# Performance work log

Hardware: AMD Instinct MI355X
Metric: run time of the kernel (lower is better)

## Reference

```python
import jax, jax.numpy as jnp
import numpy as np
import math

INPUT_SIZE = 4096
NUM_NEURONS = 4096
ATTN_SIZE = 64
BATCH = 8192


def setup_inputs() -> dict:
    key = jax.random.key(0)
    ks = jax.random.split(key, 10)
    lim_in = 1.0 / math.sqrt(INPUT_SIZE)
    lim_a = 1.0 / math.sqrt(ATTN_SIZE)
    x = jax.random.normal(ks[0], (BATCH, INPUT_SIZE), dtype=jnp.float32)
    # attention linears (torch default uniform(-1/sqrt(fan_in), ...))
    Wq = jax.random.uniform(ks[1], (ATTN_SIZE, INPUT_SIZE), jnp.float32, -lim_in, lim_in)
    bq = jnp.zeros((ATTN_SIZE,), jnp.float32)
    Wk = jax.random.uniform(ks[2], (ATTN_SIZE, INPUT_SIZE), jnp.float32, -lim_in, lim_in)
    bk = jnp.zeros((ATTN_SIZE,), jnp.float32)
    Wv = jax.random.uniform(ks[3], (ATTN_SIZE, INPUT_SIZE), jnp.float32, -lim_in, lim_in)
    bv = jnp.zeros((ATTN_SIZE,), jnp.float32)
    Wo = jax.random.uniform(ks[4], (INPUT_SIZE, ATTN_SIZE), jnp.float32, -lim_a, lim_a)
    bo = jnp.zeros((INPUT_SIZE,), jnp.float32)
    # stacked single-weight neurons: weight ~ N(0,1)*0.01, bias 0
    Wn = jax.random.normal(ks[5], (NUM_NEURONS, INPUT_SIZE), jnp.float32) * 0.01
    bn = jnp.zeros((NUM_NEURONS,), jnp.float32)
    return {"x": x, "Wq": Wq, "bq": bq, "Wk": Wk, "bk": bk,
            "Wv": Wv, "bv": bv, "Wo": Wo, "bo": bo, "Wn": Wn, "bn": bn}


def reference(x, Wq, bq, Wk, bk, Wv, bv, Wo, bo, Wn, bn):
    scale = math.sqrt(ATTN_SIZE)
    # x is treated as a length-1 "sequence" of the full feature vector: [B, 1, S]
    q = x @ Wq.T + bq            # [B, A]
    k = x @ Wk.T + bk            # [B, A]
    v = x @ Wv.T + bv            # [B, A]
    # attention over a single token: softmax of a single score == 1, kept for fidelity
    scores = jnp.sum(q * k, axis=-1, keepdims=True) / scale      # [B, 1]
    attn_w = jax.nn.softmax(scores[:, :, None], axis=-1)          # [B, 1, 1] -> all ones
    attended = attn_w[:, 0, :] * v                                # [B, A] == v
    attn_out = attended @ Wo.T + bo                               # [B, S]
    h = attn_out + x                                              # residual
    # stacked single-weight neurons == one GEMM
    out = h @ Wn.T + bn                                           # [B, N]
    return jax.nn.relu(out)
```

## Files before the change

kernel.cpp:

```cpp
#include <hip/hip_runtime.h>
#include <stdint.h>


typedef unsigned short u16;
typedef float f32x4 __attribute__((ext_vector_type(4)));
typedef __bf16 bf16x8 __attribute__((ext_vector_type(8)));
typedef u16 u16x8 __attribute__((ext_vector_type(8)));

__device__ __forceinline__ float b2f(u16 u) {
  union { unsigned int i; float f; } x; x.i = ((unsigned int)u) << 16; return x.f;
}
__device__ __forceinline__ u16 f2b(float f) {
  union { float f; unsigned int i; } x; x.f = f;
  unsigned int r = x.i + 0x7FFFu + ((x.i >> 16) & 1u);
  return (u16)(r >> 16);
}

__device__ __forceinline__ void gl_lds16(const u16* g, u16* l) {
#if __has_builtin(__builtin_amdgcn_global_load_lds)
  __builtin_amdgcn_global_load_lds((__attribute__((address_space(1))) void*)g,
                                   (__attribute__((address_space(3))) void*)l, 16, 0, 0);
#else
  int lane = threadIdx.x & 63;
  *(u16x8*)(l + lane * 8) = *(const u16x8*)g;
#endif
}

__device__ __forceinline__ f32x4 mfma16(bf16x8 a, bf16x8 b, f32x4 c) {
  return __builtin_amdgcn_mfma_f32_16x16x32_bf16(a, b, c, 0, 0, 0);
}

#define XCH 4194304L
#define WNCH 2097152L
__global__ __launch_bounds__(256) void k_cvt(
    const float* __restrict__ x, const float* __restrict__ Wn, const float* __restrict__ Wv,
    u16* __restrict__ xb, u16* __restrict__ Wnb, u16* __restrict__ Wvb) {
  long i = (long)blockIdx.x * 256 + threadIdx.x;
  const float* src; u16* dst; long off;
  if (i < XCH) { src = x; dst = xb; off = i * 8; }
  else if (i < XCH + WNCH) { src = Wn; dst = Wnb; off = (i - XCH) * 8; }
  else { src = Wv; dst = Wvb; off = (i - XCH - WNCH) * 8; }
  f32x4 a = *(const f32x4*)&src[off];
  f32x4 b = *(const f32x4*)&src[off + 4];
  u16x8 o;
#pragma unroll
  for (int e = 0; e < 4; ++e) { o[e] = f2b(a[e]); o[4 + e] = f2b(b[e]); }
  *(u16x8*)&dst[off] = o;
}

__global__ __launch_bounds__(256) void kT(const float* __restrict__ Wo, u16* __restrict__ WoT) {
  __shared__ __align__(16) u16 t[64 * 72];
  const int b = blockIdx.x;
  const int tid = threadIdx.x;
  {
    int k = tid >> 2, a0 = (tid & 3) * 16;
    const float* src = &Wo[(size_t)(b * 64 + k) * 64 + a0];
#pragma unroll
    for (int q = 0; q < 4; ++q) {
      f32x4 v = *(const f32x4*)&src[q * 4];
#pragma unroll
      for (int e = 0; e < 4; ++e) t[k * 72 + a0 + q * 4 + e] = f2b(v[e]);
    }
  }
  __syncthreads();
  {
    int a = tid >> 2, k0 = (tid & 3) * 16;
    u16x8 o0, o1;
#pragma unroll
    for (int j = 0; j < 8; ++j) o0[j] = t[(k0 + j) * 72 + a];
#pragma unroll
    for (int j = 0; j < 8; ++j) o1[j] = t[(k0 + 8 + j) * 72 + a];
    *(u16x8*)&WoT[(size_t)a * 4096 + b * 64 + k0] = o0;
    *(u16x8*)&WoT[(size_t)a * 4096 + b * 64 + k0 + 8] = o1;
  }
}

#define PBK 128
__device__ void gemm_n64(const u16* __restrict__ A, const u16* __restrict__ B,
                         u16* __restrict__ C, const float* __restrict__ bias,
                         long m0, u16* lA, u16* lB) {
  const int tid = threadIdx.x;
  const int w = tid >> 6, l = tid & 63;
  f32x4 acc[4];
#pragma unroll
  for (int nt = 0; nt < 4; ++nt) acc[nt] = (f32x4)(0.f);

  for (int k0 = 0; k0 < 4096; k0 += PBK) {
    __syncthreads();
#pragma unroll
    for (int i = 0; i < 4; ++i) {
      int row = w * 16 + i * 4 + (l >> 4);
      int p = (l & 15) ^ (i * 4 + (l >> 4));
      gl_lds16(A + (m0 + row) * (long)4096 + k0 + p * 8, lA + (w * 16 + i * 4) * PBK);
      gl_lds16(B + (long)row * 4096 + k0 + p * 8, lB + (w * 16 + i * 4) * PBK);
    }
    __syncthreads();
#pragma unroll
    for (int kk = 0; kk < 4; ++kk) {
      int slotA = ((kk * 4 + (l >> 4)) ^ (l & 15)) * 8;
      bf16x8 af = *(const bf16x8*)&lA[(w * 16 + (l & 15)) * PBK + slotA];
#pragma unroll
      for (int nt = 0; nt < 4; ++nt) {
        bf16x8 bf = *(const bf16x8*)&lB[(nt * 16 + (l & 15)) * PBK + slotA];
        acc[nt] = mfma16(af, bf, acc[nt]);
      }
    }
  }
#pragma unroll
  for (int nt = 0; nt < 4; ++nt) {
    int col = nt * 16 + (l & 15);
    float bb = bias ? bias[col] : 0.f;
#pragma unroll
    for (int r = 0; r < 4; ++r) {
      long row = m0 + w * 16 + (l >> 4) * 4 + r;
      C[row * 64 + col] = f2b(acc[nt][r] + bb);
    }
  }
}

__global__ __launch_bounds__(256, 2) void k_prep(
    const u16* __restrict__ xb, const u16* __restrict__ Wvb, const float* __restrict__ bv,
    const u16* __restrict__ Wnb, const u16* __restrict__ WoT,
    const float* __restrict__ bo, const float* __restrict__ bn,
    u16* __restrict__ V, u16* __restrict__ Wm, float* __restrict__ biasTot) {
  __shared__ __align__(16) u16 lA[64 * PBK];
  __shared__ __align__(16) u16 lB[64 * PBK];
  const int bid = blockIdx.x;
  if (bid < 128) {
    gemm_n64(xb, Wvb, V, bv, (long)bid * 64, lA, lB);
  } else if (bid < 192) {
    gemm_n64(Wnb, WoT, Wm, nullptr, (long)(bid - 128) * 64, lA, lB);
  } else {
    const int w = threadIdx.x >> 6, l = threadIdx.x & 63;
    const int n = (bid - 192) * 4 + w;
    float s = 0.f;
#pragma unroll
    for (int j = 0; j < 8; ++j) {
      int off = (j * 64 + l) * 8;
      u16x8 a = *(const u16x8*)&Wnb[(size_t)n * 4096 + off];
      f32x4 c0 = *(const f32x4*)&bo[off];
      f32x4 c1 = *(const f32x4*)&bo[off + 4];
#pragma unroll
      for (int e = 0; e < 4; ++e) s += b2f(a[e]) * c0[e] + b2f(a[4 + e]) * c1[e];
    }
#pragma unroll
    for (int o = 32; o > 0; o >>= 1) s += __shfl_xor(s, o, 64);
    if (l == 0) biasTot[n] = s + bn[n];
  }
}

__global__ __launch_bounds__(256, 2) void k_main(
    const u16* __restrict__ X, const u16* __restrict__ Wn,
    const u16* __restrict__ V, const u16* __restrict__ Wm,
    const float* __restrict__ biasTot, float* __restrict__ Out) {
  __shared__ __align__(16) u16 smem[2 * 128 * 64];
  u16* lA = smem;
  u16* lB = smem + 128 * 64;
  const int tid = threadIdx.x;
  const int w = tid >> 6, l = tid & 63;
  const int wRow = (w & 1) * 64, wCol = (w >> 1) * 64;
  const long mBase = (long)(blockIdx.x >> 5) * 128;
  const int nBase = (int)(blockIdx.x & 31) * 128;

  f32x4 acc[4][4];
#pragma unroll
  for (int mt = 0; mt < 4; ++mt)
#pragma unroll
    for (int nt = 0; nt < 4; ++nt) acc[mt][nt] = (f32x4)(0.f);

  const int srow = l >> 3;
  const int sp = ((l & 7) ^ srow) * 8;

  for (int kb = 0; kb < 65; ++kb) {
    const u16 *pA, *pB; long lda;
    if (kb < 64) { pA = X + (long)kb * 64; pB = Wn + (long)kb * 64; lda = 4096; }
    else         { pA = V;                 pB = Wm;                 lda = 64;  }
    __syncthreads();
#pragma unroll
    for (int i = 0; i < 4; ++i) {
      int row = w * 32 + i * 8 + srow;
      gl_lds16(pA + (mBase + row) * lda + sp, lA + (w * 32 + i * 8) * 64);
      gl_lds16(pB + (long)(nBase + row) * lda + sp, lB + (w * 32 + i * 8) * 64);
    }
    __syncthreads();
#pragma unroll
    for (int kk = 0; kk < 2; ++kk) {
      int slot = ((kk * 4 + (l >> 4)) ^ (l & 7)) * 8;
      bf16x8 af[4], bfr[4];
#pragma unroll
      for (int mt = 0; mt < 4; ++mt)
        af[mt] = *(const bf16x8*)&lA[(wRow + mt * 16 + (l & 15)) * 64 + slot];
#pragma unroll
      for (int nt = 0; nt < 4; ++nt)
        bfr[nt] = *(const bf16x8*)&lB[(wCol + nt * 16 + (l & 15)) * 64 + slot];
#pragma unroll
      for (int mt = 0; mt < 4; ++mt)
#pragma unroll
        for (int nt = 0; nt < 4; ++nt) acc[mt][nt] = mfma16(af[mt], bfr[nt], acc[mt][nt]);
    }
  }

  __syncthreads();
  float* eb = ((float*)smem) + w * 1024;
#pragma unroll
  for (int mt = 0; mt < 4; ++mt) {
#pragma unroll
    for (int nt = 0; nt < 4; ++nt) {
      float bt = biasTot[nBase + wCol + nt * 16 + (l & 15)];
#pragma unroll
      for (int r = 0; r < 4; ++r) {
        float val = acc[mt][nt][r] + bt;
        eb[((l >> 4) * 4 + r) * 64 + nt * 16 + (l & 15)] = fmaxf(val, 0.f);
      }
    }
    int rr = l >> 2, c0 = (l & 3) * 16;
    long grow = mBase + wRow + mt * 16 + rr;
    int gcol = nBase + wCol + c0;
    f32x4 o0 = *(const f32x4*)&eb[rr * 64 + c0];
    f32x4 o1 = *(const f32x4*)&eb[rr * 64 + c0 + 4];
    f32x4 o2 = *(const f32x4*)&eb[rr * 64 + c0 + 8];
    f32x4 o3 = *(const f32x4*)&eb[rr * 64 + c0 + 12];
    *(f32x4*)&Out[grow * 4096 + gcol] = o0;
    *(f32x4*)&Out[grow * 4096 + gcol + 4] = o1;
    *(f32x4*)&Out[grow * 4096 + gcol + 8] = o2;
    *(f32x4*)&Out[grow * 4096 + gcol + 12] = o3;
  }
}

extern "C" void kernel_launch(void* const* d_in, const int* in_sizes, int n_in,
                              void* d_out, int out_size, void* d_ws, size_t ws_size,
                              hipStream_t stream) {
  const float* x  = (const float*)d_in[0];
  const float* Wv = (const float*)d_in[5];
  const float* bv = (const float*)d_in[6];
  const float* Wo = (const float*)d_in[7];
  const float* bo = (const float*)d_in[8];
  const float* Wn = (const float*)d_in[9];
  const float* bn = (const float*)d_in[10];
  float* out = (float*)d_out;

  char* ws = (char*)d_ws;
  u16* xb  = (u16*)ws;
  u16* Wnb = (u16*)(ws + (64L << 20));
  u16* Wvb = (u16*)(ws + (96L << 20));
  u16* WoT = (u16*)(ws + (96L << 20) + (512 << 10));
  u16* V   = (u16*)(ws + (97L << 20));
  u16* Wm  = (u16*)(ws + (98L << 20));
  float* biasTot = (float*)(ws + (98L << 20) + (512 << 10));

  k_cvt<<<dim3(24704), dim3(256), 0, stream>>>(x, Wn, Wv, xb, Wnb, Wvb);
  kT<<<dim3(64), dim3(256), 0, stream>>>(Wo, WoT);
  k_prep<<<dim3(1216), dim3(256), 0, stream>>>(xb, Wvb, bv, Wnb, WoT, bo, bn, V, Wm, biasTot);
  k_main<<<dim3(2048), dim3(256), 0, stream>>>(xb, Wnb, V, Wm, biasTot, out);
}
```

Measured before the change: 605.9 us.

## Materialize residual h in bf16 instead of folding Wo into Wn

Drops the Wm = Wn·Wo precompute and the extra K=64 block in the main GEMM. Instead it computes V with a split-K kernel that converts x and Wv in-kernel, writing fp32 partials into the output buffer. It then builds h = V·Wo^T + bo + x in bf16 and runs the main GEMM on h with only bn as bias. This removes the separate x conversion pass and the Wn·WoT GEMM, but adds an extra bf16 write and read of h and rounds h to bf16 rather than x.

```diff
diff --git a/kernel.cpp b/kernel.cpp
--- a/kernel.cpp
+++ b/kernel.cpp
@@ -7,9 +7,6 @@
 typedef __bf16 bf16x8 __attribute__((ext_vector_type(8)));
 typedef u16 u16x8 __attribute__((ext_vector_type(8)));
 
-__device__ __forceinline__ float b2f(u16 u) {
-  union { unsigned int i; float f; } x; x.i = ((unsigned int)u) << 16; return x.f;
-}
 __device__ __forceinline__ u16 f2b(float f) {
   union { float f; unsigned int i; } x; x.f = f;
   unsigned int r = x.i + 0x7FFFu + ((x.i >> 16) & 1u);
@@ -30,129 +27,158 @@
   return __builtin_amdgcn_mfma_f32_16x16x32_bf16(a, b, c, 0, 0, 0);
 }
 
-#define XCH 4194304L
-#define WNCH 2097152L
-__global__ __launch_bounds__(256) void k_cvt(
-    const float* __restrict__ x, const float* __restrict__ Wn, const float* __restrict__ Wv,
-    u16* __restrict__ xb, u16* __restrict__ Wnb, u16* __restrict__ Wvb) {
-  long i = (long)blockIdx.x * 256 + threadIdx.x;
-  const float* src; u16* dst; long off;
-  if (i < XCH) { src = x; dst = xb; off = i * 8; }
-  else if (i < XCH + WNCH) { src = Wn; dst = Wnb; off = (i - XCH) * 8; }
-  else { src = Wv; dst = Wvb; off = (i - XCH - WNCH) * 8; }
-  f32x4 a = *(const f32x4*)&src[off];
-  f32x4 b = *(const f32x4*)&src[off + 4];
-  u16x8 o;
-#pragma unroll
-  for (int e = 0; e < 4; ++e) { o[e] = f2b(a[e]); o[4 + e] = f2b(b[e]); }
-  *(u16x8*)&dst[off] = o;
-}
-
-__global__ __launch_bounds__(256) void kT(const float* __restrict__ Wo, u16* __restrict__ WoT) {
-  __shared__ __align__(16) u16 t[64 * 72];
-  const int b = blockIdx.x;
-  const int tid = threadIdx.x;
-  {
-    int k = tid >> 2, a0 = (tid & 3) * 16;
-    const float* src = &Wo[(size_t)(b * 64 + k) * 64 + a0];
-#pragma unroll
-    for (int q = 0; q < 4; ++q) {
-      f32x4 v = *(const f32x4*)&src[q * 4];
-#pragma unroll
-      for (int e = 0; e < 4; ++e) t[k * 72 + a0 + q * 4 + e] = f2b(v[e]);
-    }
-  }
-  __syncthreads();
-  {
-    int a = tid >> 2, k0 = (tid & 3) * 16;
-    u16x8 o0, o1;
-#pragma unroll
-    for (int j = 0; j < 8; ++j) o0[j] = t[(k0 + j) * 72 + a];
-#pragma unroll
-    for (int j = 0; j < 8; ++j) o1[j] = t[(k0 + 8 + j) * 72 + a];
-    *(u16x8*)&WoT[(size_t)a * 4096 + b * 64 + k0] = o0;
-    *(u16x8*)&WoT[(size_t)a * 4096 + b * 64 + k0 + 8] = o1;
-  }
-}
-
-#define PBK 128
-__device__ void gemm_n64(const u16* __restrict__ A, const u16* __restrict__ B,
-                         u16* __restrict__ C, const float* __restrict__ bias,
-                         long m0, u16* lA, u16* lB) {
+__device__ __forceinline__ void cvt16(const float* s, u16* d0, u16* d1) {
+  f32x4 a0 = *(const f32x4*)s, a1 = *(const f32x4*)(s + 4);
+  f32x4 a2 = *(const f32x4*)(s + 8), a3 = *(const f32x4*)(s + 12);
+  u16x8 o0, o1;
+#pragma unroll
+  for (int e = 0; e < 4; ++e) { o0[e] = f2b(a0[e]); o0[4 + e] = f2b(a1[e]); }
+#pragma unroll
+  for (int e = 0; e < 4; ++e) { o1[e] = f2b(a2[e]); o1[4 + e] = f2b(a3[e]); }
+  *(u16x8*)d0 = o0; *(u16x8*)d1 = o1;
+}
+
+__global__ __launch_bounds__(256, 2) void k_v(
+    const float* __restrict__ x, const float* __restrict__ Wv, float* __restrict__ Vp) {
+  __shared__ __align__(16) u16 lA[64 * 72];
+  __shared__ __align__(16) u16 lB[64 * 72];
   const int tid = threadIdx.x;
   const int w = tid >> 6, l = tid & 63;
+  const long m0 = (long)(blockIdx.x >> 2) * 64;
+  const int kbase = (int)(blockIdx.x & 3) * 1024;
   f32x4 acc[4];
 #pragma unroll
   for (int nt = 0; nt < 4; ++nt) acc[nt] = (f32x4)(0.f);
 
-  for (int k0 = 0; k0 < 4096; k0 += PBK) {
-    __syncthreads();
-#pragma unroll
-    for (int i = 0; i < 4; ++i) {
-      int row = w * 16 + i * 4 + (l >> 4);
-      int p = (l & 15) ^ (i * 4 + (l >> 4));
-      gl_lds16(A + (m0 + row) * (long)4096 + k0 + p * 8, lA + (w * 16 + i * 4) * PBK);
-      gl_lds16(B + (long)row * 4096 + k0 + p * 8, lB + (w * 16 + i * 4) * PBK);
-    }
-    __syncthreads();
-#pragma unroll
-    for (int kk = 0; kk < 4; ++kk) {
-      int slotA = ((kk * 4 + (l >> 4)) ^ (l & 15)) * 8;
-      bf16x8 af = *(const bf16x8*)&lA[(w * 16 + (l & 15)) * PBK + slotA];
+  const int srow = tid >> 2, sc = (tid & 3) * 16;
+  for (int it = 0; it < 16; ++it) {
+    const int k0 = kbase + it * 64;
+    __syncthreads();
+    cvt16(&x[(m0 + srow) * 4096 + k0 + sc], &lA[srow * 72 + sc], &lA[srow * 72 + sc + 8]);
+    cvt16(&Wv[(long)srow * 4096 + k0 + sc], &lB[srow * 72 + sc], &lB[srow * 72 + sc + 8]);
+    __syncthreads();
+#pragma unroll
+    for (int kk = 0; kk < 2; ++kk) {
+      const int ko = kk * 32 + (l >> 4) * 8;
+      bf16x8 af = *(const bf16x8*)&lA[(w * 16 + (l & 15)) * 72 + ko];
 #pragma unroll
       for (int nt = 0; nt < 4; ++nt) {
-        bf16x8 bf = *(const bf16x8*)&lB[(nt * 16 + (l & 15)) * PBK + slotA];
+        bf16x8 bf = *(const bf16x8*)&lB[(nt * 16 + (l & 15)) * 72 + ko];
         acc[nt] = mfma16(af, bf, acc[nt]);
       }
     }
   }
+  const long ksoff = (long)(blockIdx.x & 3) * 8192;
 #pragma unroll
   for (int nt = 0; nt < 4; ++nt) {
     int col = nt * 16 + (l & 15);
-    float bb = bias ? bias[col] : 0.f;
 #pragma unroll
     for (int r = 0; r < 4; ++r) {
       long row = m0 + w * 16 + (l >> 4) * 4 + r;
-      C[row * 64 + col] = f2b(acc[nt][r] + bb);
-    }
-  }
-}
-
-__global__ __launch_bounds__(256, 2) void k_prep(
-    const u16* __restrict__ xb, const u16* __restrict__ Wvb, const float* __restrict__ bv,
-    const u16* __restrict__ Wnb, const u16* __restrict__ WoT,
-    const float* __restrict__ bo, const float* __restrict__ bn,
-    u16* __restrict__ V, u16* __restrict__ Wm, float* __restrict__ biasTot) {
-  __shared__ __align__(16) u16 lA[64 * PBK];
-  __shared__ __align__(16) u16 lB[64 * PBK];
-  const int bid = blockIdx.x;
-  if (bid < 128) {
-    gemm_n64(xb, Wvb, V, bv, (long)bid * 64, lA, lB);
-  } else if (bid < 192) {
-    gemm_n64(Wnb, WoT, Wm, nullptr, (long)(bid - 128) * 64, lA, lB);
-  } else {
-    const int w = threadIdx.x >> 6, l = threadIdx.x & 63;
-    const int n = (bid - 192) * 4 + w;
-    float s = 0.f;
-#pragma unroll
-    for (int j = 0; j < 8; ++j) {
-      int off = (j * 64 + l) * 8;
-      u16x8 a = *(const u16x8*)&Wnb[(size_t)n * 4096 + off];
-      f32x4 c0 = *(const f32x4*)&bo[off];
-      f32x4 c1 = *(const f32x4*)&bo[off + 4];
-#pragma unroll
-      for (int e = 0; e < 4; ++e) s += b2f(a[e]) * c0[e] + b2f(a[4 + e]) * c1[e];
-    }
-#pragma unroll
-    for (int o = 32; o > 0; o >>= 1) s += __shfl_xor(s, o, 64);
-    if (l == 0) biasTot[n] = s + bn[n];
+      Vp[(ksoff + row) * 64 + col] = acc[nt][r];
+    }
+  }
+}
+
+__global__ __launch_bounds__(256) void k_cvtWn(const float* __restrict__ Wn,
+                                               u16* __restrict__ Wnb) {
+  long off = ((long)blockIdx.x * 256 + threadIdx.x) * 8;
+  f32x4 a = *(const f32x4*)&Wn[off];
+  f32x4 b = *(const f32x4*)&Wn[off + 4];
+  u16x8 o;
+#pragma unroll
+  for (int e = 0; e < 4; ++e) { o[e] = f2b(a[e]); o[4 + e] = f2b(b[e]); }
+  *(u16x8*)&Wnb[off] = o;
+}
+
+__global__ __launch_bounds__(256, 3) void k_h(
+    const float* __restrict__ x, const float* __restrict__ Wo,
+    const float* __restrict__ bv, const float* __restrict__ bo,
+    const float* __restrict__ Vp, u16* __restrict__ hb) {
+  __shared__ __align__(16) u16 smem[64 * 72 + 256 * 72];
+  u16* lV = smem;
+  u16* lW = smem + 64 * 72;
+  const int tid = threadIdx.x;
+  const int w = tid >> 6, l = tid & 63;
+  const long m0 = (long)(blockIdx.x >> 4) * 64;
+  const int c0 = (int)(blockIdx.x & 15) * 256;
+
+  {
+    int row = tid >> 2, a0 = (tid & 3) * 16;
+    f32x4 s[4];
+#pragma unroll
+    for (int j = 0; j < 4; ++j) s[j] = *(const f32x4*)&Vp[(m0 + row) * 64 + a0 + j * 4];
+#pragma unroll
+    for (int ks = 1; ks < 4; ++ks)
+#pragma unroll
+      for (int j = 0; j < 4; ++j)
+        s[j] += *(const f32x4*)&Vp[((long)ks * 8192 + m0 + row) * 64 + a0 + j * 4];
+#pragma unroll
+    for (int j = 0; j < 4; ++j) s[j] += *(const f32x4*)&bv[a0 + j * 4];
+    u16x8 o0, o1;
+#pragma unroll
+    for (int e = 0; e < 4; ++e) { o0[e] = f2b(s[0][e]); o0[4 + e] = f2b(s[1][e]); }
+#pragma unroll
+    for (int e = 0; e < 4; ++e) { o1[e] = f2b(s[2][e]); o1[4 + e] = f2b(s[3][e]); }
+    *(u16x8*)&lV[row * 72 + a0] = o0;
+    *(u16x8*)&lV[row * 72 + a0 + 8] = o1;
+  }
+#pragma unroll
+  for (int g = 0; g < 4; ++g) {
+    int row = g * 64 + (tid >> 2), cc = (tid & 3) * 16;
+    cvt16(&Wo[(long)(c0 + row) * 64 + cc], &lW[row * 72 + cc], &lW[row * 72 + cc + 8]);
+  }
+  __syncthreads();
+
+  f32x4 acc[16];
+#pragma unroll
+  for (int nt = 0; nt < 16; ++nt) acc[nt] = (f32x4)(0.f);
+#pragma unroll
+  for (int kk = 0; kk < 2; ++kk) {
+    const int ko = kk * 32 + (l >> 4) * 8;
+    bf16x8 af = *(const bf16x8*)&lV[(w * 16 + (l & 15)) * 72 + ko];
+#pragma unroll
+    for (int nt = 0; nt < 16; ++nt) {
+      bf16x8 bf = *(const bf16x8*)&lW[(nt * 16 + (l & 15)) * 72 + ko];
+      acc[nt] = mfma16(af, bf, acc[nt]);
+    }
+  }
+  __syncthreads();
+
+  float* eb = ((float*)smem) + w * 1024;
+#pragma unroll
+  for (int g = 0; g < 4; ++g) {
+#pragma unroll
+    for (int q = 0; q < 4; ++q) {
+      int nt = g * 4 + q;
+#pragma unroll
+      for (int r = 0; r < 4; ++r)
+        eb[((l >> 4) * 4 + r) * 64 + q * 16 + (l & 15)] = acc[nt][r];
+    }
+    int rr = l >> 2, cc = (l & 3) * 16;
+    long grow = m0 + w * 16 + rr;
+    int gcol = c0 + g * 64 + cc;
+    f32x4 h0 = *(const f32x4*)&eb[rr * 64 + cc];
+    f32x4 h1 = *(const f32x4*)&eb[rr * 64 + cc + 4];
+    f32x4 h2 = *(const f32x4*)&eb[rr * 64 + cc + 8];
+    f32x4 h3 = *(const f32x4*)&eb[rr * 64 + cc + 12];
+    h0 += *(const f32x4*)&x[grow * 4096 + gcol]     + *(const f32x4*)&bo[gcol];
+    h1 += *(const f32x4*)&x[grow * 4096 + gcol + 4] + *(const f32x4*)&bo[gcol + 4];
+    h2 += *(const f32x4*)&x[grow * 4096 + gcol + 8] + *(const f32x4*)&bo[gcol + 8];
+    h3 += *(const f32x4*)&x[grow * 4096 + gcol + 12] + *(const f32x4*)&bo[gcol + 12];
+    u16x8 o0, o1;
+#pragma unroll
+    for (int e = 0; e < 4; ++e) { o0[e] = f2b(h0[e]); o0[4 + e] = f2b(h1[e]); }
+#pragma unroll
+    for (int e = 0; e < 4; ++e) { o1[e] = f2b(h2[e]); o1[4 + e] = f2b(h3[e]); }
+    *(u16x8*)&hb[grow * 4096 + gcol] = o0;
+    *(u16x8*)&hb[grow * 4096 + gcol + 8] = o1;
   }
 }
 
 __global__ __launch_bounds__(256, 2) void k_main(
     const u16* __restrict__ X, const u16* __restrict__ Wn,
-    const u16* __restrict__ V, const u16* __restrict__ Wm,
-    const float* __restrict__ biasTot, float* __restrict__ Out) {
+    const float* __restrict__ bn, float* __restrict__ Out) {
   __shared__ __align__(16) u16 smem[2 * 128 * 64];
   u16* lA = smem;
   u16* lB = smem + 128 * 64;
@@ -171,16 +197,15 @@
   const int srow = l >> 3;
   const int sp = ((l & 7) ^ srow) * 8;
 
-  for (int kb = 0; kb < 65; ++kb) {
-    const u16 *pA, *pB; long lda;
-    if (kb < 64) { pA = X + (long)kb * 64; pB = Wn + (long)kb * 64; lda = 4096; }
-    else         { pA = V;                 pB = Wm;                 lda = 64;  }
+  for (int kb = 0; kb < 64; ++kb) {
+    const u16* pA = X + (long)kb * 64;
+    const u16* pB = Wn + (long)kb * 64;
     __syncthreads();
 #pragma unroll
     for (int i = 0; i < 4; ++i) {
       int row = w * 32 + i * 8 + srow;
-      gl_lds16(pA + (mBase + row) * lda + sp, lA + (w * 32 + i * 8) * 64);
-      gl_lds16(pB + (long)(nBase + row) * lda + sp, lB + (w * 32 + i * 8) * 64);
+      gl_lds16(pA + (mBase + row) * (long)4096 + sp, lA + (w * 32 + i * 8) * 64);
+      gl_lds16(pB + (long)(nBase + row) * 4096 + sp, lB + (w * 32 + i * 8) * 64);
     }
     __syncthreads();
 #pragma unroll
@@ -206,7 +231,7 @@
   for (int mt = 0; mt < 4; ++mt) {
 #pragma unroll
     for (int nt = 0; nt < 4; ++nt) {
-      float bt = biasTot[nBase + wCol + nt * 16 + (l & 15)];
+      float bt = bn[nBase + wCol + nt * 16 + (l & 15)];
 #pragma unroll
       for (int r = 0; r < 4; ++r) {
         float val = acc[mt][nt][r] + bt;
@@ -240,16 +265,12 @@
   float* out = (float*)d_out;
 
   char* ws = (char*)d_ws;
-  u16* xb  = (u16*)ws;
+  u16* hb  = (u16*)ws;
   u16* Wnb = (u16*)(ws + (64L << 20));
-  u16* Wvb = (u16*)(ws + (96L << 20));
-  u16* WoT = (u16*)(ws + (96L << 20) + (512 << 10));
-  u16* V   = (u16*)(ws + (97L << 20));
-  u16* Wm  = (u16*)(ws + (98L << 20));
-  float* biasTot = (float*)(ws + (98L << 20) + (512 << 10));
-
-  k_cvt<<<dim3(24704), dim3(256), 0, stream>>>(x, Wn, Wv, xb, Wnb, Wvb);
-  kT<<<dim3(64), dim3(256), 0, stream>>>(Wo, WoT);
-  k_prep<<<dim3(1216), dim3(256), 0, stream>>>(xb, Wvb, bv, Wnb, WoT, bo, bn, V, Wm, biasTot);
-  k_main<<<dim3(2048), dim3(256), 0, stream>>>(xb, Wnb, V, Wm, biasTot, out);
-}
+  float* Vp = (float*)d_out;
+
+  k_v<<<dim3(512), dim3(256), 0, stream>>>(x, Wv, Vp);
+  k_cvtWn<<<dim3(8192), dim3(256), 0, stream>>>(Wn, Wnb);
+  k_h<<<dim3(2048), dim3(256), 0, stream>>>(x, Wo, bv, bo, Vp, hb);
+  k_main<<<dim3(2048), dim3(256), 0, stream>>>(hb, Wnb, bn, out);
+}
```

New measurement: 606.8 us. About the same (+0.1%).
